# Kernel optimization log

Hardware: AMD Instinct MI355X
Metric: run time of the kernel (lower is better)

Reference implementation:

```python
import jax, jax.numpy as jnp
import numpy as np
from jax import lax

NEG = -1e9  # effective -inf, safe for fp32 and for gradients


def asg_loss(inputs, transitions, targets):
    """ASG criterion (wav2letter / gtn_applications semantics).

    inputs:      [B, T, N] emissions (log scores)
    transitions: [N+1, N]; transitions[0, i] = start score of class i,
                 transitions[i+1, j] = score of transition j -> i
    targets:     [B, L] int class ids (already replabel-packed + garbage-interleaved)
    Returns mean over batch of (logZ - forced_align_score) / L.
    """
    B, T, N = inputs.shape
    L = targets.shape[1]
    init = transitions[0]      # [N]
    trans = transitions[1:]    # [N, N], trans[i, j]: j -> i

    # ---- denominator: free recursion over all label sequences ----
    alpha0 = inputs[:, 0, :] + init  # [B, N]
    emis_t = jnp.swapaxes(inputs, 0, 1)  # [T, B, N]

    def den_step(alpha, e_t):
        # alpha[b, j] -> new alpha[b, i] = e_t[b, i] + LSE_j(alpha[b, j] + trans[i, j])
        a = jax.nn.logsumexp(alpha[:, None, :] + trans[None, :, :], axis=-1) + e_t
        return a, None

    alphaT, _ = lax.scan(den_step, alpha0, emis_t[1:])
    logZ = jax.nn.logsumexp(alphaT, axis=-1)  # [B]

    # ---- numerator: forced-alignment graph (self-loop or advance) ----
    # emissions gathered at target labels: [B, T, L]
    emis_y = jnp.take_along_axis(inputs, jnp.broadcast_to(targets[:, None, :], (B, T, L)), axis=2)
    stay_w = trans[targets, targets]                      # [B, L]   y_s -> y_s
    adv_w = trans[targets[:, 1:], targets[:, :-1]]        # [B, L-1] y_{s-1} -> y_s

    beta0 = jnp.full((B, L), NEG, dtype=inputs.dtype)
    beta0 = beta0.at[:, 0].set(init[targets[:, 0]] + emis_y[:, 0, 0])
    emis_y_t = jnp.swapaxes(emis_y, 0, 1)  # [T, B, L]

    def num_step(beta, e_t):
        stay = beta + stay_w
        adv = jnp.concatenate(
            [jnp.full((B, 1), NEG, dtype=beta.dtype), beta[:, :-1] + adv_w], axis=1)
        b = jnp.logaddexp(stay, adv) + e_t
        return b, None

    betaT, _ = lax.scan(num_step, beta0, emis_y_t[1:])
    target_score = betaT[:, -1]  # must end having consumed all L labels

    # reduction = 'mean': scale each sample by 1/len(target), then batch mean
    return jnp.mean((logZ - target_score) / L)


def setup_inputs() -> dict:
    key = jax.random.key(0)
    k1, k2, k3 = jax.random.split(key, 3)
    B, T, N, L = 128, 4000, 64, 101
    inputs = jax.random.normal(k1, (B, T, N), dtype=jnp.float32)
    transitions = jax.random.normal(k2, (N + 1, N), dtype=jnp.float32) * 0.1
    targets = jax.random.randint(k3, (B, L), 0, N, dtype=jnp.int64)
    return {"inputs": inputs, "transitions": transitions, "targets": targets}


def reference(inputs, transitions, targets):
    return asg_loss(inputs, transitions, targets)
```

## Files before the change

kernel.cpp:

```cpp
#include <hip/hip_runtime.h>


#define TT 4000
#define NN 64
#define LL 101
#define NSEG 32

static constexpr float L2E  = 1.44269504088896340736f;
static constexpr float LN2F = 0.69314718055994530942f;
static constexpr float NEG2 = -1.0e30f;

#define WS_X    0
#define WS_NF   4096
#define WS_HB   18432
#define WS_LOSS 32768

#if defined(__has_builtin)
#if __has_builtin(__builtin_amdgcn_mfma_f32_16x16x16bf16_1k)
#define BF16MM 1
#endif
#if __has_builtin(__builtin_amdgcn_exp2f)
#define FEXP2(x) __builtin_amdgcn_exp2f(x)
#endif
#if __has_builtin(__builtin_amdgcn_logf)
#define FLOG2(x) __builtin_amdgcn_logf(x)
#endif
#endif
#ifndef FEXP2
#define FEXP2(x) exp2f(x)
#endif
#ifndef FLOG2
#define FLOG2(x) log2f(x)
#endif

typedef float f32x4 __attribute__((ext_vector_type(4)));
typedef short s16x4 __attribute__((ext_vector_type(4)));
typedef _Float16 h4 __attribute__((ext_vector_type(4)));

__device__ __forceinline__ unsigned cvt2(float a, float b) {
#ifdef BF16MM
  const unsigned ua = __builtin_bit_cast(unsigned, a);
  const unsigned ub = __builtin_bit_cast(unsigned, b);
  const unsigned ra = (ua + 0x7FFFu + ((ua >> 16) & 1u)) >> 16;
  const unsigned rb = (ub + 0x7FFFu + ((ub >> 16) & 1u)) >> 16;
  return ra | (rb << 16);
#else
  return __builtin_bit_cast(unsigned,
      __builtin_amdgcn_cvt_pkrtz(fminf(a, 3.0e4f), fminf(b, 3.0e4f)));
#endif
}

__device__ __forceinline__ f32x4 MM(uint2 a, uint2 b, f32x4 c) {
#ifdef BF16MM
  return __builtin_amdgcn_mfma_f32_16x16x16bf16_1k(
      __builtin_bit_cast(s16x4, a), __builtin_bit_cast(s16x4, b), c, 0, 0, 0);
#else
  return __builtin_amdgcn_mfma_f32_16x16x16f16(
      __builtin_bit_cast(h4, a), __builtin_bit_cast(h4, b), c, 0, 0, 0);
#endif
}

template<int CTRL>
__device__ __forceinline__ float dppf(float x) {
  return __builtin_bit_cast(float, __builtin_amdgcn_update_dpp(
      0, __builtin_bit_cast(int, x), CTRL, 0xf, 0xf, true));
}

template<int DIR>
__device__ __forceinline__ void num_chain(const float* __restrict__ em,
                                          const float* __restrict__ TR,
                                          const int* __restrict__ Y,
                                          float* __restrict__ ws,
                                          const int b, const int l)
{
  const bool v0 = (2 * l     <= 100);
  const bool v1 = (2 * l + 1 <= 100);
  const int k0 = v0 ? 2 * l     : 100;
  const int k1 = v1 ? 2 * l + 1 : 100;
  const int y0 = Y[b * LL + k0];
  const int y1 = Y[b * LL + k1];
  const float SW0 = v0 ? FEXP2(TR[(y0 + 1) * NN + y0] * L2E) : 0.f;
  const float SW1 = v1 ? FEXP2(TR[(y1 + 1) * NN + y1] * L2E) : 0.f;
  float WLOC, WRECV, B0, B1, C;
  bool recvok;
  if (DIR == 0) {
    WLOC = v1 ? FEXP2(TR[(y1 + 1) * NN + y0] * L2E) : 0.f;
    const int ym0 = Y[b * LL + (k0 > 0 ? k0 - 1 : 0)];
    recvok = v0 && (l > 0);
    WRECV = recvok ? FEXP2(TR[(y0 + 1) * NN + ym0] * L2E) : 0.f;
    B0 = (l == 0) ? 1.f : 0.f;
    B1 = 0.f;
    C  = (l == 0) ? (TR[y0] + em[y0]) * L2E : 0.f;
  } else {
    WLOC = v1 ? FEXP2(TR[(y1 + 1) * NN + y0] * L2E) : 0.f;
    const int kp = (2 * l + 2 <= 100) ? 2 * l + 2 : 100;
    const int yp1 = Y[b * LL + kp];
    recvok = (2 * l + 2 <= 100);
    WRECV = recvok ? FEXP2(TR[(yp1 + 1) * NN + y1] * L2E) : 0.f;
    B0 = (l == 50) ? 1.f : 0.f;
    B1 = 0.f;
    C  = (l == 50) ? em[(size_t)(TT - 1) * NN + y0] * L2E : 0.f;
  }

#define TROW(t) ((size_t)((DIR == 0) ? (t) : (TT - 1 - (t))) * NN)

  float RA[16], RB[16], RC[16];
  float PC0[16], PC1[16];
  float PN0[16], PN1[16];
  float ADJ = 0.f;

#define ISSUE(R, e)                                                            \
  { _Pragma("unroll") for (int k_ = 0; k_ < 16; ++k_) {                        \
      int t_ = 1 + 16 * (e) + k_; t_ = (t_ < 1999) ? t_ : 1999;                \
      R[k_] = em[TROW(t_) + l]; } }

#define PROC(P0, P1, R)                                                        \
  { _Pragma("unroll") for (int k_ = 0; k_ < 16; ++k_) {                        \
      const float r_ = R[k_];                                                  \
      const float a_ = __shfl(r_, y0);                                         \
      const float b_ = __shfl(r_, y1);                                         \
      P0[k_] = FEXP2(a_ * L2E);                                                \
      P1[k_] = FEXP2(b_ * L2E); } }

#define COPYP()                                                                \
  { _Pragma("unroll") for (int k_ = 0; k_ < 16; ++k_) {                        \
      PC0[k_] = PN0[k_]; PC1[k_] = PN1[k_]; } }

#define RESCALE()                                                              \
  {                                                                            \
    const float v_ = B0 + B1;                                                  \
    const int bits_ = __builtin_bit_cast(int, v_);                             \
    const int m_ = (v_ > 0.f) ? ((bits_ >> 23) & 255) - 127 : 0;               \
    const float sc_ = __builtin_bit_cast(float, (127 - m_) << 23);             \
    B0 *= sc_; B1 *= sc_; C += (float)m_;                                      \
    const float Cn_ = dppf<(DIR == 0) ? 0x138 : 0x130>(C);                     \
    const float dC_ = fminf(fmaxf(Cn_ - C, -120.f), 120.f);                    \
    ADJ = recvok ? FEXP2(dC_) * WRECV : 0.f;                                   \
  }

#define NSTEP2(E0v, E1v)                                                       \
  {                                                                            \
    if (DIR == 0) {                                                            \
      const float NB = dppf<0x138>(B1);                                        \
      const float t0 = fmaf(NB, ADJ, B0 * SW0);                                \
      const float t1 = fmaf(B0, WLOC, B1 * SW1);                               \
      B0 = t0 * (E0v); B1 = t1 * (E1v);                                        \
    } else {                                                                   \
      const float NB = dppf<0x130>(B0);                                        \
      const float t1 = fmaf(NB, ADJ, B1 * SW1);                                \
      const float t0 = fmaf(B1, WLOC, B0 * SW0);                               \
      B0 = t0 * (E0v); B1 = t1 * (E1v);                                        \
    }                                                                          \
  }

#define RUN16()                                                                \
  { RESCALE();                                                                 \
    _Pragma("unroll") for (int k_ = 0; k_ < 8; ++k_)                           \
      NSTEP2(PC0[k_], PC1[k_]);                                                \
    RESCALE();                                                                 \
    _Pragma("unroll") for (int k_ = 8; k_ < 16; ++k_)                          \
      NSTEP2(PC0[k_], PC1[k_]); }

#define PHASE(e, Rslot)                                                        \
  { RUN16();                                                                   \
    COPYP();                                                                   \
    PROC(PN0, PN1, Rslot);                                                     \
    ISSUE(Rslot, (e) + 5); }

  ISSUE(RA, 0); ISSUE(RB, 1); ISSUE(RC, 2);
  PROC(PC0, PC1, RA);  ISSUE(RA, 3);
  PROC(PN0, PN1, RB);  ISSUE(RB, 4);

  for (int s = 0; s < 41; ++s) {
    const int e = 3 * s;
    PHASE(e,     RC);
    PHASE(e + 1, RA);
    PHASE(e + 2, RB);
  }
  RUN16();
  COPYP();
  RESCALE();
#pragma unroll
  for (int k_ = 0; k_ < 8; ++k_) NSTEP2(PC0[k_], PC1[k_]);
  RESCALE();
#pragma unroll
  for (int k_ = 8; k_ < 15; ++k_) NSTEP2(PC0[k_], PC1[k_]);

#undef PHASE
#undef RUN16
#undef NSTEP2
#undef RESCALE
#undef COPYP
#undef PROC
#undef ISSUE
#undef TROW

  const float o0 = (B0 > 1e-37f) ? C + FLOG2(B0) : NEG2;
  const float o1 = (B1 > 1e-37f) ? C + FLOG2(B1) : NEG2;
  const int base = (DIR ? WS_HB : WS_NF) + b * 112;
  if (v0) ws[base + 2 * l]     = o0;
  if (v1) ws[base + 2 * l + 1] = o1;
}

__global__ __launch_bounds__(128) void asg_main(
    const float* __restrict__ E, const float* __restrict__ TR,
    const int* __restrict__ Y, float* __restrict__ ws)
{
  const int bid  = blockIdx.x;
  const int w    = threadIdx.x >> 6;
  const int lane = threadIdx.x & 63;
  const int b    = bid >> 1;
  const float* em = E + (size_t)b * TT * NN;

  if (w == 0) {
    const int h = bid & 1;
    const int c = lane & 15, g = lane >> 4;
    const int j = h * 16 + c;

    uint2 Af[4][4];
#pragma unroll
    for (int rt = 0; rt < 4; ++rt)
#pragma unroll
      for (int kt = 0; kt < 4; ++kt) {
        const float* tr = TR + (size_t)(16 * rt + c + 1) * NN + 16 * kt + 4 * g;
        const float w0 = FEXP2(tr[0] * L2E), w1 = FEXP2(tr[1] * L2E);
        const float w2 = FEXP2(tr[2] * L2E), w3 = FEXP2(tr[3] * L2E);
        Af[rt][kt].x = cvt2(w0, w1);
        Af[rt][kt].y = cvt2(w2, w3);
      }

    f32x4 P[4];
#pragma unroll
    for (int rt = 0; rt < 4; ++rt)
#pragma unroll
      for (int e = 0; e < 4; ++e) {
        const int row = 16 * rt + 4 * g + e;
        P[rt][e] = (j == 0) ? FEXP2((em[row] + TR[row]) * L2E) : 1.0f;
      }

    float Csum = 0.f, snap31 = 0.f;
    const float* ebase = em + (size_t)(124 * j + 1) * NN + 4 * g;

#define COLSUM(dst) { float t_ =                                               \
      (P[0].x + P[0].y + P[0].z + P[0].w) + (P[1].x + P[1].y + P[1].z + P[1].w)\
    + (P[2].x + P[2].y + P[2].z + P[2].w) + (P[3].x + P[3].y + P[3].z + P[3].w);\
    t_ += __shfl_xor(t_, 16); t_ += __shfl_xor(t_, 32);                        \
    (dst) = fmaxf(t_, 1e-30f); }

#define RENORM() { float cs_; COLSUM(cs_);                                     \
    const int mb_ = ((__builtin_bit_cast(int, cs_) >> 23) & 255) - 127;        \
    const float sc_ = __builtin_bit_cast(float, (127 - mb_) << 23);            \
    P[0] *= sc_; P[1] *= sc_; P[2] *= sc_; P[3] *= sc_;                        \
    Csum += (float)mb_; }

#define ELOAD(D, s_) { const int se_ = (s_) < 154 ? (s_) : 154;                \
    const f32x4* p_ = (const f32x4*)(ebase + (size_t)se_ * NN);                \
    D[0] = p_[0]; D[1] = p_[4]; D[2] = p_[8]; D[3] = p_[12]; }

#define STEP(M)                                                                \
    {                                                                          \
      uint2 Bf[4];                                                             \
      _Pragma("unroll") for (int kt = 0; kt < 4; ++kt) {                       \
        Bf[kt].x = cvt2(P[kt].x, P[kt].y);                                     \
        Bf[kt].y = cvt2(P[kt].z, P[kt].w);                                     \
      }                                                                        \
      _Pragma("unroll") for (int rt = 0; rt < 4; ++rt) {                       \
        f32x4 acc = {0.f, 0.f, 0.f, 0.f};                                      \
        acc = MM(Af[rt][0], Bf[0], acc);                                       \
        acc = MM(Af[rt][1], Bf[1], acc);                                       \
        acc = MM(Af[rt][2], Bf[2], acc);                                       \
        acc = MM(Af[rt][3], Bf[3], acc);                                       \
        _Pragma("unroll") for (int e = 0; e < 4; ++e)                          \
          P[rt][e] = fminf(fmaxf(                                              \
              acc[e] * FEXP2(fmaf(M[rt][e], L2E, -6.7f)), 1e-20f), 1e25f);     \
      }                                                                        \
    }

#define SUB(Ebuf, ss, kr)                                                      \
    { f32x4 T_[4] = {Ebuf[0], Ebuf[1], Ebuf[2], Ebuf[3]};                      \
      ELOAD(Ebuf, (ss) + 6);                                                   \
      STEP(T_);                                                                \
      if ((ss) == 30) { float cs2_; COLSUM(cs2_);                              \
                        snap31 = Csum + FLOG2(cs2_) + 6.7f * 31.f; }           \
      if ((kr) == 5) RENORM(); }

    f32x4 E0[4], E1[4], E2[4], E3[4], E4[4], E5[4];
    ELOAD(E0, 0); ELOAD(E1, 1); ELOAD(E2, 2);
    ELOAD(E3, 3); ELOAD(E4, 4); ELOAD(E5, 5);

    for (int it = 0; it < 25; ++it) {
      const int s = 6 * it;
      SUB(E0, s, 0);     SUB(E1, s + 1, 1); SUB(E2, s + 2, 2);
      SUB(E3, s + 3, 3); SUB(E4, s + 4, 4); SUB(E5, s + 5, 5);
    }
    { f32x4 T_[4] = {E0[0], E0[1], E0[2], E0[3]}; STEP(T_); }
    { f32x4 T_[4] = {E1[0], E1[1], E1[2], E1[3]}; STEP(T_); }
    { f32x4 T_[4] = {E2[0], E2[1], E2[2], E2[3]}; STEP(T_); }
    { f32x4 T_[4] = {E3[0], E3[1], E3[2], E3[3]}; STEP(T_); }
    { f32x4 T_[4] = {E4[0], E4[1], E4[2], E4[3]}; STEP(T_); }

    float csf; COLSUM(csf);
    const float fin = Csum + FLOG2(csf) + 6.7f * 155.f;
    const float X = fin - ((j == 0) ? 0.f : snap31);
    if (lane < 16) ws[WS_X + b * NSEG + (h * 16 + lane)] = X;

#undef SUB
#undef STEP
#undef ELOAD
#undef RENORM
#undef COLSUM

  } else {
    const int dir = bid & 1;
    if (dir == 0) num_chain<0>(em, TR, Y, ws, b, lane);
    else          num_chain<1>(em, TR, Y, ws, b, lane);
  }
}

__global__ __launch_bounds__(128) void asg_combine(
    const float* __restrict__ TR, const int* __restrict__ Y,
    const float* __restrict__ ws, float* __restrict__ lossv)
{
  const int b = blockIdx.x;
  const int tid = threadIdx.x;
  __shared__ float sN[LL], sH[LL], red[128];
  __shared__ float sLogZ;

  if (tid == 0) {
    float z = 0.f;
    for (int s = 0; s < NSEG; ++s) z += ws[WS_X + b * NSEG + s];
    sLogZ = z;
  }
  if (tid < LL) { sN[tid] = ws[WS_NF + b * 112 + tid]; sH[tid] = ws[WS_HB + b * 112 + tid]; }
  __syncthreads();

  float val2 = -3.0e38f;
  if (tid < LL) {
    const int l = tid;
    const int y = Y[b * LL + l];
    const float s1 = sN[l] + TR[(y + 1) * NN + y] * L2E;
    float s2 = NEG2;
    if (l > 0) {
      const int ymm = Y[b * LL + l - 1];
      s2 = sN[l - 1] + TR[(y + 1) * NN + ymm] * L2E;
    }
    const float m = fmaxf(s1, s2);
    val2 = m + log2f(exp2f(s1 - m) + exp2f(s2 - m)) + sH[l];
  }
  red[tid] = val2;
  __syncthreads();
  if (tid == 0) {
    float m = red[0];
    for (int k = 1; k < LL; ++k) m = fmaxf(m, red[k]);
    float s = 0.f;
    for (int k = 0; k < LL; ++k) s += exp2f(red[k] - m);
    const float tgt2 = m + log2f(s);
    lossv[b] = (sLogZ - tgt2) * LN2F / (float)LL;
  }
}

__global__ __launch_bounds__(64) void asg_reduce(const float* __restrict__ lossv,
                                                 float* __restrict__ out)
{
  const int tid = threadIdx.x;
  float v = lossv[tid] + lossv[tid + 64];
  for (int off = 32; off; off >>= 1) v += __shfl_xor(v, off);
  if (tid == 0) out[0] = v * (1.0f / 128.0f);
}

extern "C" void kernel_launch(void* const* d_in, const int* in_sizes, int n_in,
                              void* d_out, int out_size, void* d_ws, size_t ws_size,
                              hipStream_t stream) {
  const float* E  = (const float*)d_in[0];
  const float* TR = (const float*)d_in[1];
  const int*   Y  = (const int*)d_in[2];
  float* out = (float*)d_out;
  float* ws  = (float*)d_ws;
  float* lossv = ws + WS_LOSS;

  asg_main<<<dim3(256), dim3(128), 0, stream>>>(E, TR, Y, ws);
  asg_combine<<<dim3(128), dim3(128), 0, stream>>>(TR, Y, ws, lossv);
  asg_reduce<<<dim3(1), dim3(64), 0, stream>>>(lossv, out);
}
```

Measured before the change: 131.2 us.

## Split denominator and numerator into separate kernels, doubling time segments

The fused kernel that ran the denominator MFMA wave and the numerator chain wave together is split into two launches. The denominator now uses 64 time segments of 62 steps across four waves per batch, which shortens its serial chain. The numerator is rewritten around a 48-entry register ring with an 8-step lookahead of exponentials in place of the triple-buffer copy scheme. In exchange there is one more kernel launch, the two kernels run back to back on the stream rather than concurrently, and more segment partials have to be combined.

```diff
diff --git a/kernel.cpp b/kernel.cpp
--- a/kernel.cpp
+++ b/kernel.cpp
@@ -4,16 +4,18 @@
 #define TT 4000
 #define NN 64
 #define LL 101
-#define NSEG 32
+#define NSEG 64
+#define SEGN 62
+#define SLOTS 93
 
 static constexpr float L2E  = 1.44269504088896340736f;
 static constexpr float LN2F = 0.69314718055994530942f;
 static constexpr float NEG2 = -1.0e30f;
 
 #define WS_X    0
-#define WS_NF   4096
-#define WS_HB   18432
-#define WS_LOSS 32768
+#define WS_NF   8192
+#define WS_HB   22528
+#define WS_LOSS 36864
 
 #if defined(__has_builtin)
 #if __has_builtin(__builtin_amdgcn_mfma_f32_16x16x16bf16_1k)
@@ -64,6 +66,111 @@
 __device__ __forceinline__ float dppf(float x) {
   return __builtin_bit_cast(float, __builtin_amdgcn_update_dpp(
       0, __builtin_bit_cast(int, x), CTRL, 0xf, 0xf, true));
+}
+
+__global__ __launch_bounds__(128) void asg_den(
+    const float* __restrict__ E, const float* __restrict__ TR,
+    float* __restrict__ ws)
+{
+  const int bid  = blockIdx.x;
+  const int w    = threadIdx.x >> 6;
+  const int lane = threadIdx.x & 63;
+  const int b    = bid >> 1;
+  const int p    = bid & 1;
+  const int g4   = p * 2 + w;
+  const float* em = E + (size_t)b * TT * NN;
+
+  const int c = lane & 15, g = lane >> 4;
+  const int j = g4 * 16 + c;
+
+  uint2 Af[4][4];
+#pragma unroll
+  for (int rt = 0; rt < 4; ++rt)
+#pragma unroll
+    for (int kt = 0; kt < 4; ++kt) {
+      const float* tr = TR + (size_t)(16 * rt + c + 1) * NN + 16 * kt + 4 * g;
+      Af[rt][kt].x = cvt2(FEXP2(tr[0] * L2E), FEXP2(tr[1] * L2E));
+      Af[rt][kt].y = cvt2(FEXP2(tr[2] * L2E), FEXP2(tr[3] * L2E));
+    }
+
+  f32x4 P[4];
+#pragma unroll
+  for (int rt = 0; rt < 4; ++rt)
+#pragma unroll
+    for (int e = 0; e < 4; ++e) {
+      const int row = 16 * rt + 4 * g + e;
+      P[rt][e] = (j == 0) ? FEXP2((em[row] + TR[row]) * L2E) : 1.0f;
+    }
+
+  float Csum = 0.f, snap = 0.f;
+  const float* ebase = em + (size_t)(SEGN * j + 1) * NN + 4 * g;
+
+#define COLSUM(dst) { float t_ =                                               \
+    (P[0].x + P[0].y + P[0].z + P[0].w) + (P[1].x + P[1].y + P[1].z + P[1].w)  \
+  + (P[2].x + P[2].y + P[2].z + P[2].w) + (P[3].x + P[3].y + P[3].z + P[3].w); \
+  t_ += __shfl_xor(t_, 16); t_ += __shfl_xor(t_, 32);                          \
+  (dst) = fmaxf(t_, 1e-30f); }
+
+#define RENORM() { float cs_; COLSUM(cs_);                                     \
+  const int mb_ = ((__builtin_bit_cast(int, cs_) >> 23) & 255) - 127;          \
+  const float sc_ = __builtin_bit_cast(float, (127 - mb_) << 23);              \
+  P[0] *= sc_; P[1] *= sc_; P[2] *= sc_; P[3] *= sc_;                          \
+  Csum += (float)mb_; }
+
+#define ELOAD(D, s_) { const int se_ = (s_) < (SLOTS - 1) ? (s_) : (SLOTS - 1);\
+  const f32x4* p_ = (const f32x4*)(ebase + (size_t)se_ * NN);                  \
+  D[0] = p_[0]; D[1] = p_[4]; D[2] = p_[8]; D[3] = p_[12]; }
+
+#define STEP(M)                                                                \
+  {                                                                            \
+    uint2 Bf[4];                                                               \
+    _Pragma("unroll") for (int kt = 0; kt < 4; ++kt) {                         \
+      Bf[kt].x = cvt2(P[kt].x, P[kt].y);                                       \
+      Bf[kt].y = cvt2(P[kt].z, P[kt].w);                                       \
+    }                                                                          \
+    _Pragma("unroll") for (int rt = 0; rt < 4; ++rt) {                         \
+      f32x4 acc = {0.f, 0.f, 0.f, 0.f};                                        \
+      acc = MM(Af[rt][0], Bf[0], acc);                                         \
+      acc = MM(Af[rt][1], Bf[1], acc);                                         \
+      acc = MM(Af[rt][2], Bf[2], acc);                                         \
+      acc = MM(Af[rt][3], Bf[3], acc);                                         \
+      _Pragma("unroll") for (int e = 0; e < 4; ++e)                            \
+        P[rt][e] = fminf(fmaxf(                                                \
+            acc[e] * FEXP2(fmaf(M[rt][e], L2E, -6.7f)), 1e-20f), 1e25f);       \
+    }                                                                          \
+  }
+
+#define SUB(Ebuf, ss, kr)                                                      \
+  { f32x4 T_[4] = {Ebuf[0], Ebuf[1], Ebuf[2], Ebuf[3]};                        \
+    ELOAD(Ebuf, (ss) + 6);                                                     \
+    STEP(T_);                                                                  \
+    if ((ss) == 30) { float cs2_; COLSUM(cs2_);                                \
+                      snap = Csum + FLOG2(cs2_) + 6.7f * 31.f; }               \
+    if ((kr) == 5) RENORM(); }
+
+  f32x4 E0[4], E1[4], E2[4], E3[4], E4[4], E5[4];
+  ELOAD(E0, 0); ELOAD(E1, 1); ELOAD(E2, 2);
+  ELOAD(E3, 3); ELOAD(E4, 4); ELOAD(E5, 5);
+
+  for (int it = 0; it < 15; ++it) {
+    const int s = 6 * it;
+    SUB(E0, s, 0);     SUB(E1, s + 1, 1); SUB(E2, s + 2, 2);
+    SUB(E3, s + 3, 3); SUB(E4, s + 4, 4); SUB(E5, s + 5, 5);
+  }
+  { f32x4 T_[4] = {E0[0], E0[1], E0[2], E0[3]}; STEP(T_); }
+  { f32x4 T_[4] = {E1[0], E1[1], E1[2], E1[3]}; STEP(T_); }
+  { f32x4 T_[4] = {E2[0], E2[1], E2[2], E2[3]}; STEP(T_); }
+
+  float csf; COLSUM(csf);
+  const float fin = Csum + FLOG2(csf) + 6.7f * (float)SLOTS;
+  const float X = fin - ((j == 0) ? 0.f : snap);
+  if (lane < 16) ws[WS_X + b * NSEG + g4 * 16 + lane] = X;
+
+#undef SUB
+#undef STEP
+#undef ELOAD
+#undef RENORM
+#undef COLSUM
 }
 
 template<int DIR>
@@ -103,28 +210,11 @@
   }
 
 #define TROW(t) ((size_t)((DIR == 0) ? (t) : (TT - 1 - (t))) * NN)
-
-  float RA[16], RB[16], RC[16];
-  float PC0[16], PC1[16];
-  float PN0[16], PN1[16];
+#define RADDR(t) em[TROW(((t) < 1999 ? (t) : 1999)) + l]
+
+  float ring[48];
+  float PE0[16], PE1[16];
   float ADJ = 0.f;
-
-#define ISSUE(R, e)                                                            \
-  { _Pragma("unroll") for (int k_ = 0; k_ < 16; ++k_) {                        \
-      int t_ = 1 + 16 * (e) + k_; t_ = (t_ < 1999) ? t_ : 1999;                \
-      R[k_] = em[TROW(t_) + l]; } }
-
-#define PROC(P0, P1, R)                                                        \
-  { _Pragma("unroll") for (int k_ = 0; k_ < 16; ++k_) {                        \
-      const float r_ = R[k_];                                                  \
-      const float a_ = __shfl(r_, y0);                                         \
-      const float b_ = __shfl(r_, y1);                                         \
-      P0[k_] = FEXP2(a_ * L2E);                                                \
-      P1[k_] = FEXP2(b_ * L2E); } }
-
-#define COPYP()                                                                \
-  { _Pragma("unroll") for (int k_ = 0; k_ < 16; ++k_) {                        \
-      PC0[k_] = PN0[k_]; PC1[k_] = PN1[k_]; } }
 
 #define RESCALE()                                                              \
   {                                                                            \
@@ -153,46 +243,43 @@
     }                                                                          \
   }
 
-#define RUN16()                                                                \
-  { RESCALE();                                                                 \
-    _Pragma("unroll") for (int k_ = 0; k_ < 8; ++k_)                           \
-      NSTEP2(PC0[k_], PC1[k_]);                                                \
-    RESCALE();                                                                 \
-    _Pragma("unroll") for (int k_ = 8; k_ < 16; ++k_)                          \
-      NSTEP2(PC0[k_], PC1[k_]); }
-
-#define PHASE(e, Rslot)                                                        \
-  { RUN16();                                                                   \
-    COPYP();                                                                   \
-    PROC(PN0, PN1, Rslot);                                                     \
-    ISSUE(Rslot, (e) + 5); }
-
-  ISSUE(RA, 0); ISSUE(RB, 1); ISSUE(RC, 2);
-  PROC(PC0, PC1, RA);  ISSUE(RA, 3);
-  PROC(PN0, PN1, RB);  ISSUE(RB, 4);
-
-  for (int s = 0; s < 41; ++s) {
-    const int e = 3 * s;
-    PHASE(e,     RC);
-    PHASE(e + 1, RA);
-    PHASE(e + 2, RB);
-  }
-  RUN16();
-  COPYP();
-  RESCALE();
-#pragma unroll
-  for (int k_ = 0; k_ < 8; ++k_) NSTEP2(PC0[k_], PC1[k_]);
-  RESCALE();
-#pragma unroll
-  for (int k_ = 8; k_ < 15; ++k_) NSTEP2(PC0[k_], PC1[k_]);
-
-#undef PHASE
-#undef RUN16
+#pragma unroll
+  for (int k = 0; k < 48; ++k) ring[(1 + k) % 48] = RADDR(1 + k);
+#pragma unroll
+  for (int t = 1; t <= 8; ++t) {
+    const float r_ = ring[t % 48];
+    PE0[t & 15] = FEXP2(__shfl(r_, y0) * L2E);
+    PE1[t & 15] = FEXP2(__shfl(r_, y1) * L2E);
+  }
+
+#define QSTEP(k)                                                               \
+  { if (((k) & 7) == 0) RESCALE();                                             \
+    NSTEP2(PE0[(1 + (k)) & 15], PE1[(1 + (k)) & 15]);                          \
+    { const float r_ = ring[(1 + (k) + 8) % 48];                               \
+      PE0[(1 + (k) + 8) & 15] = FEXP2(__shfl(r_, y0) * L2E);                   \
+      PE1[(1 + (k) + 8) & 15] = FEXP2(__shfl(r_, y1) * L2E); }                 \
+    ring[(1 + (k)) % 48] = RADDR(tc + (k) + 48); }
+
+#define Q4(k0)  QSTEP(k0) QSTEP((k0) + 1) QSTEP((k0) + 2) QSTEP((k0) + 3)
+#define Q16(k0) Q4(k0) Q4((k0) + 4) Q4((k0) + 8) Q4((k0) + 12)
+
+  for (int i = 0; i < 41; ++i) {
+    const int tc = 1 + 48 * i;
+    Q16(0) Q16(16) Q16(32)
+  }
+  {
+    const int tc = 1969;
+    Q16(0)
+    Q4(16) Q4(20) Q4(24)
+    QSTEP(28) QSTEP(29) QSTEP(30)
+  }
+
+#undef Q16
+#undef Q4
+#undef QSTEP
 #undef NSTEP2
 #undef RESCALE
-#undef COPYP
-#undef PROC
-#undef ISSUE
+#undef RADDR
 #undef TROW
 
   const float o0 = (B0 > 1e-37f) ? C + FLOG2(B0) : NEG2;
@@ -202,119 +289,16 @@
   if (v1) ws[base + 2 * l + 1] = o1;
 }
 
-__global__ __launch_bounds__(128) void asg_main(
+__global__ __launch_bounds__(64) void asg_num(
     const float* __restrict__ E, const float* __restrict__ TR,
     const int* __restrict__ Y, float* __restrict__ ws)
 {
-  const int bid  = blockIdx.x;
-  const int w    = threadIdx.x >> 6;
-  const int lane = threadIdx.x & 63;
-  const int b    = bid >> 1;
+  const int bid = blockIdx.x;
+  const int b   = bid >> 1;
+  const int dir = bid & 1;
   const float* em = E + (size_t)b * TT * NN;
-
-  if (w == 0) {
-    const int h = bid & 1;
-    const int c = lane & 15, g = lane >> 4;
-    const int j = h * 16 + c;
-
-    uint2 Af[4][4];
-#pragma unroll
-    for (int rt = 0; rt < 4; ++rt)
-#pragma unroll
-      for (int kt = 0; kt < 4; ++kt) {
-        const float* tr = TR + (size_t)(16 * rt + c + 1) * NN + 16 * kt + 4 * g;
-        const float w0 = FEXP2(tr[0] * L2E), w1 = FEXP2(tr[1] * L2E);
-        const float w2 = FEXP2(tr[2] * L2E), w3 = FEXP2(tr[3] * L2E);
-        Af[rt][kt].x = cvt2(w0, w1);
-        Af[rt][kt].y = cvt2(w2, w3);
-      }
-
-    f32x4 P[4];
-#pragma unroll
-    for (int rt = 0; rt < 4; ++rt)
-#pragma unroll
-      for (int e = 0; e < 4; ++e) {
-        const int row = 16 * rt + 4 * g + e;
-        P[rt][e] = (j == 0) ? FEXP2((em[row] + TR[row]) * L2E) : 1.0f;
-      }
-
-    float Csum = 0.f, snap31 = 0.f;
-    const float* ebase = em + (size_t)(124 * j + 1) * NN + 4 * g;
-
-#define COLSUM(dst) { float t_ =                                               \
-      (P[0].x + P[0].y + P[0].z + P[0].w) + (P[1].x + P[1].y + P[1].z + P[1].w)\
-    + (P[2].x + P[2].y + P[2].z + P[2].w) + (P[3].x + P[3].y + P[3].z + P[3].w);\
-    t_ += __shfl_xor(t_, 16); t_ += __shfl_xor(t_, 32);                        \
-    (dst) = fmaxf(t_, 1e-30f); }
-
-#define RENORM() { float cs_; COLSUM(cs_);                                     \
-    const int mb_ = ((__builtin_bit_cast(int, cs_) >> 23) & 255) - 127;        \
-    const float sc_ = __builtin_bit_cast(float, (127 - mb_) << 23);            \
-    P[0] *= sc_; P[1] *= sc_; P[2] *= sc_; P[3] *= sc_;                        \
-    Csum += (float)mb_; }
-
-#define ELOAD(D, s_) { const int se_ = (s_) < 154 ? (s_) : 154;                \
-    const f32x4* p_ = (const f32x4*)(ebase + (size_t)se_ * NN);                \
-    D[0] = p_[0]; D[1] = p_[4]; D[2] = p_[8]; D[3] = p_[12]; }
-
-#define STEP(M)                                                                \
-    {                                                                          \
-      uint2 Bf[4];                                                             \
-      _Pragma("unroll") for (int kt = 0; kt < 4; ++kt) {                       \
-        Bf[kt].x = cvt2(P[kt].x, P[kt].y);                                     \
-        Bf[kt].y = cvt2(P[kt].z, P[kt].w);                                     \
-      }                                                                        \
-      _Pragma("unroll") for (int rt = 0; rt < 4; ++rt) {                       \
-        f32x4 acc = {0.f, 0.f, 0.f, 0.f};                                      \
-        acc = MM(Af[rt][0], Bf[0], acc);                                       \
-        acc = MM(Af[rt][1], Bf[1], acc);                                       \
-        acc = MM(Af[rt][2], Bf[2], acc);                                       \
-        acc = MM(Af[rt][3], Bf[3], acc);                                       \
-        _Pragma("unroll") for (int e = 0; e < 4; ++e)                          \
-          P[rt][e] = fminf(fmaxf(                                              \
-              acc[e] * FEXP2(fmaf(M[rt][e], L2E, -6.7f)), 1e-20f), 1e25f);     \
-      }                                                                        \
-    }
-
-#define SUB(Ebuf, ss, kr)                                                      \
-    { f32x4 T_[4] = {Ebuf[0], Ebuf[1], Ebuf[2], Ebuf[3]};                      \
-      ELOAD(Ebuf, (ss) + 6);                                                   \
-      STEP(T_);                                                                \
-      if ((ss) == 30) { float cs2_; COLSUM(cs2_);                              \
-                        snap31 = Csum + FLOG2(cs2_) + 6.7f * 31.f; }           \
-      if ((kr) == 5) RENORM(); }
-
-    f32x4 E0[4], E1[4], E2[4], E3[4], E4[4], E5[4];
-    ELOAD(E0, 0); ELOAD(E1, 1); ELOAD(E2, 2);
-    ELOAD(E3, 3); ELOAD(E4, 4); ELOAD(E5, 5);
-
-    for (int it = 0; it < 25; ++it) {
-      const int s = 6 * it;
-      SUB(E0, s, 0);     SUB(E1, s + 1, 1); SUB(E2, s + 2, 2);
-      SUB(E3, s + 3, 3); SUB(E4, s + 4, 4); SUB(E5, s + 5, 5);
-    }
-    { f32x4 T_[4] = {E0[0], E0[1], E0[2], E0[3]}; STEP(T_); }
-    { f32x4 T_[4] = {E1[0], E1[1], E1[2], E1[3]}; STEP(T_); }
-    { f32x4 T_[4] = {E2[0], E2[1], E2[2], E2[3]}; STEP(T_); }
-    { f32x4 T_[4] = {E3[0], E3[1], E3[2], E3[3]}; STEP(T_); }
-    { f32x4 T_[4] = {E4[0], E4[1], E4[2], E4[3]}; STEP(T_); }
-
-    float csf; COLSUM(csf);
-    const float fin = Csum + FLOG2(csf) + 6.7f * 155.f;
-    const float X = fin - ((j == 0) ? 0.f : snap31);
-    if (lane < 16) ws[WS_X + b * NSEG + (h * 16 + lane)] = X;
-
-#undef SUB
-#undef STEP
-#undef ELOAD
-#undef RENORM
-#undef COLSUM
-
-  } else {
-    const int dir = bid & 1;
-    if (dir == 0) num_chain<0>(em, TR, Y, ws, b, lane);
-    else          num_chain<1>(em, TR, Y, ws, b, lane);
-  }
+  if (dir == 0) num_chain<0>(em, TR, Y, ws, b, (int)threadIdx.x);
+  else          num_chain<1>(em, TR, Y, ws, b, (int)threadIdx.x);
 }
 
 __global__ __launch_bounds__(128) void asg_combine(
@@ -378,7 +362,8 @@
   float* ws  = (float*)d_ws;
   float* lossv = ws + WS_LOSS;
 
-  asg_main<<<dim3(256), dim3(128), 0, stream>>>(E, TR, Y, ws);
+  asg_den<<<dim3(256), dim3(128), 0, stream>>>(E, TR, ws);
+  asg_num<<<dim3(256), dim3(64), 0, stream>>>(E, TR, Y, ws);
   asg_combine<<<dim3(128), dim3(128), 0, stream>>>(TR, Y, ws, lossv);
   asg_reduce<<<dim3(1), dim3(64), 0, stream>>>(lossv, out);
 }
```

New measurement: 153.0 us. +16.6%, slower.
